# Kernel tuning notes

Measured on AMD Instinct MI355X. Metric: run time of the kernel, lower is better.

The kernel has to match this reference:

```python
import jax, jax.numpy as jnp
import numpy as np
from jax import lax

T, S, H, A = 1024, 1024, 2048, 128


def setup_inputs() -> dict:
    key = jax.random.key(0)
    ks = jax.random.split(key, 11)
    sc = 0.02  # small init scale to keep gates in a reasonable range
    rn = lambda k, shp: jax.random.normal(k, shp, dtype=jnp.float32) * sc
    return {
        "x": jax.random.normal(ks[0], (T, S), dtype=jnp.float32),
        "W_ih1": rn(ks[1], (4 * H, S)),
        "W_hh1": rn(ks[2], (4 * H, H)),
        "b_ih1": rn(ks[3], (4 * H,)),
        "b_hh1": rn(ks[4], (4 * H,)),
        "W_ih2": rn(ks[5], (4 * H, H)),
        "W_hh2": rn(ks[6], (4 * H, H)),
        "b_ih2": rn(ks[7], (4 * H,)),
        "b_hh2": rn(ks[8], (4 * H,)),
        "W_lin": rn(ks[9], (A, H)),
        "b_lin": rn(ks[10], (A,)),
    }


def _lstm_cell(xt, h, c, W_ih, W_hh, b):
    # PyTorch LSTMCell: gates ordered (i, f, g, o)
    gates = xt @ W_ih.T + h @ W_hh.T + b  # [4H]
    i, f, g, o = jnp.split(gates, 4)
    c_new = jax.nn.sigmoid(f) * c + jax.nn.sigmoid(i) * jnp.tanh(g)
    h_new = jax.nn.sigmoid(o) * jnp.tanh(c_new)
    return h_new, c_new


def reference(x, W_ih1, W_hh1, b_ih1, b_hh1, W_ih2, W_hh2, b_ih2, b_hh2, W_lin, b_lin):
    Hd = W_hh1.shape[1]
    b1 = b_ih1 + b_hh1
    b2 = b_ih2 + b_hh2

    def step(carry, xt):
        h1, c1, h2, c2 = carry
        h1, c1 = _lstm_cell(xt, h1, c1, W_ih1, W_hh1, b1)
        h2, c2 = _lstm_cell(h1, h2, c2, W_ih2, W_hh2, b2)
        return (h1, c1, h2, c2), None

    z = jnp.zeros((Hd,), dtype=x.dtype)
    (h1, c1, h2, c2), _ = lax.scan(step, (z, z, z, z), x)
    # linear head on final h of layer 2; batch==1 so [-1] == the single row
    return h2 @ W_lin.T + b_lin  # [A]
```

## Files before the change

kernel.cpp:

```cpp
#include <hip/hip_runtime.h>

#define T_ 1024
#define S_ 1024
#define H_ 2048
#define A_ 128
#define NBLK 256
#define THR 256

typedef __attribute__((ext_vector_type(8))) short short8;
typedef __attribute__((ext_vector_type(4))) float f32x4;

__device__ __forceinline__ float sigmf(float v) { return 1.0f / (1.0f + __expf(-v)); }

__device__ __forceinline__ ushort f2bf(float f) {
    uint u = __float_as_uint(f);
    return (ushort)((u + 0x7fffu + ((u >> 16) & 1u)) >> 16);
}

__device__ __forceinline__ short8 pack8(const float* __restrict__ s) {
    const float4 f0 = *(const float4*)(s);
    const float4 f1 = *(const float4*)(s + 4);
    uint4 o;
    o.x = (uint)f2bf(f0.x) | ((uint)f2bf(f0.y) << 16);
    o.y = (uint)f2bf(f0.z) | ((uint)f2bf(f0.w) << 16);
    o.z = (uint)f2bf(f1.x) | ((uint)f2bf(f1.y) << 16);
    o.w = (uint)f2bf(f1.z) | ((uint)f2bf(f1.w) << 16);
    return __builtin_bit_cast(short8, o);
}

__device__ __forceinline__ void poll8(const uint* __restrict__ p, uint tag, uint* g) {
    for (;;) {
#pragma unroll
        for (int i = 0; i < 8; ++i)
            g[i] = __hip_atomic_load(p + i, __ATOMIC_RELAXED, __HIP_MEMORY_SCOPE_AGENT);
        uint bad = 0;
#pragma unroll
        for (int i = 0; i < 8; ++i) bad |= (g[i] >> 16) ^ tag;
        if (bad == 0) return;
        __builtin_amdgcn_s_sleep(1);
    }
}

__device__ __forceinline__ void pack_hc(const uint* g, ushort* dst) {
    uint4 o;
    o.x = (g[0] & 0xffffu) | (g[1] << 16); o.y = (g[2] & 0xffffu) | (g[3] << 16);
    o.z = (g[4] & 0xffffu) | (g[5] << 16); o.w = (g[6] & 0xffffu) | (g[7] << 16);
    *(uint4*)dst = o;
}

__global__ void cvt_bf16(const float* __restrict__ src,
                         ushort* __restrict__ dst, int n4) {
    int i = blockIdx.x * blockDim.x + threadIdx.x;
    const int stride = gridDim.x * blockDim.x;
    for (; i < n4; i += stride) {
        const uint4 u = reinterpret_cast<const uint4*>(src)[i];
        ushort4 o;
        uint a;
        a = u.x; o.x = (ushort)((a + 0x7fffu + ((a >> 16) & 1u)) >> 16);
        a = u.y; o.y = (ushort)((a + 0x7fffu + ((a >> 16) & 1u)) >> 16);
        a = u.z; o.z = (ushort)((a + 0x7fffu + ((a >> 16) & 1u)) >> 16);
        a = u.w; o.w = (ushort)((a + 0x7fffu + ((a >> 16) & 1u)) >> 16);
        reinterpret_cast<ushort4*>(dst)[i] = o;
    }
}

__global__ __launch_bounds__(256, 2) void gemm_x1(
    const ushort* __restrict__ Abf, const ushort* __restrict__ Bbf,
    const float* __restrict__ bih1, const float* __restrict__ bhh1,
    float* __restrict__ X1) {
    __shared__ ushort At[64][80];
    __shared__ ushort Bt[64][80];
    const int tx = threadIdx.x;
    const int w = tx >> 6, lane = tx & 63;
    const int row0 = blockIdx.x * 64;
    const int col0 = blockIdx.y * 64;
    f32x4 acc[4];
#pragma unroll
    for (int n4 = 0; n4 < 4; ++n4) { acc[n4][0] = 0.f; acc[n4][1] = 0.f; acc[n4][2] = 0.f; acc[n4][3] = 0.f; }
    const int sr = tx >> 2, sc = (tx & 3) * 16;
    for (int k0 = 0; k0 < 1024; k0 += 64) {
        const uint4 a0 = *(const uint4*)(Abf + (size_t)(row0 + sr) * 1024 + k0 + sc);
        const uint4 a1 = *(const uint4*)(Abf + (size_t)(row0 + sr) * 1024 + k0 + sc + 8);
        const uint4 b0 = *(const uint4*)(Bbf + (size_t)(col0 + sr) * 1024 + k0 + sc);
        const uint4 b1 = *(const uint4*)(Bbf + (size_t)(col0 + sr) * 1024 + k0 + sc + 8);
        __syncthreads();
        *(uint4*)(&At[sr][sc]) = a0;
        *(uint4*)(&At[sr][sc + 8]) = a1;
        *(uint4*)(&Bt[sr][sc]) = b0;
        *(uint4*)(&Bt[sr][sc + 8]) = b1;
        __syncthreads();
#pragma unroll
        for (int kk = 0; kk < 64; kk += 32) {
            short8 af = *(const short8*)(&At[16 * w + (lane & 15)][kk + (lane >> 4) * 8]);
#pragma unroll
            for (int n4 = 0; n4 < 4; ++n4) {
                short8 bf = *(const short8*)(&Bt[n4 * 16 + (lane & 15)][kk + (lane >> 4) * 8]);
                acc[n4] = __builtin_amdgcn_mfma_f32_16x16x32_bf16(af, bf, acc[n4], 0, 0, 0);
            }
        }
    }
#pragma unroll
    for (int n4 = 0; n4 < 4; ++n4) {
        const int col = col0 + n4 * 16 + (lane & 15);
        const float bias = bih1[col] + bhh1[col];
#pragma unroll
        for (int r = 0; r < 4; ++r) {
            const int rowv = row0 + 16 * w + (lane >> 4) * 4 + r;
            X1[(size_t)rowv * 8192 + col] = acc[n4][r] + bias;
        }
    }
}

__global__ __launch_bounds__(THR, 1) void lstm_mfma(
    const float* __restrict__ X1,
    const float* __restrict__ Whh1,
    const float* __restrict__ W2i, const float* __restrict__ W2h,
    const float* __restrict__ bih2, const float* __restrict__ bhh2,
    const float* __restrict__ Wlin, const float* __restrict__ blin,
    uint* __restrict__ hp1, uint* __restrict__ hp2,
    float* __restrict__ out)
{
    __shared__ ushort hc[4096];
    __shared__ float pl[4][64];

    const int b = blockIdx.x, tid = threadIdx.x;
    const int w = tid >> 6, lane = tid & 63;
    const int j0 = b * 8;
    const int m = lane & 15;
    const int ko = (lane >> 4) * 8;

    short8 a1[2][16];
#pragma unroll
    for (int g = 0; g < 2; ++g) {
        const int r = g * 16 + m;
        const int R = (r & 3) * H_ + j0 + (r >> 2);
        const float* src = Whh1 + (size_t)R * H_ + w * 512 + ko;
#pragma unroll
        for (int c = 0; c < 16; ++c)
            a1[g][c] = pack8(src + c * 32);
    }
    short8 a2[2][32];
#pragma unroll
    for (int g = 0; g < 2; ++g) {
        const int r = g * 16 + m;
        const int R = (r & 3) * H_ + j0 + (r >> 2);
        const float* base = (w < 2) ? (W2i + (size_t)R * H_ + w * 1024 + ko)
                                    : (W2h + (size_t)R * H_ + (w - 2) * 1024 + ko);
#pragma unroll
        for (int c = 0; c < 32; ++c)
            a2[g][c] = pack8(base + c * 32);
    }

    float c1 = 0.f, c2 = 0.f;
    float b2g[4] = {0.f, 0.f, 0.f, 0.f};
    if (tid >= 8 && tid < 16) {
        const int jl = tid - 8;
#pragma unroll
        for (int g = 0; g < 4; ++g) {
            const int R = g * H_ + j0 + jl;
            b2g[g] = bih2[R] + bhh2[R];
        }
    }

#pragma unroll 1
    for (int t = 0; t <= T_; ++t) {
        float xg[4] = {0.f, 0.f, 0.f, 0.f};
        if (tid < 8 && t < T_) {
#pragma unroll
            for (int g = 0; g < 4; ++g)
                xg[g] = X1[(size_t)t * 8192 + g * H_ + j0 + tid];
        }

        {
            uint g0[8];
            if (t >= 1) {
                const uint* p = hp1 + ((((t - 1) & 1) * 256 + tid) << 4);
                poll8(p, (uint)(t - 1) & 0xffffu, g0);
            } else {
#pragma unroll
                for (int i = 0; i < 8; ++i) g0[i] = 0u;
            }
            pack_hc(g0, hc + tid * 8);
        }
        __syncthreads();

        if (t < T_) {
            f32x4 acc0, acc1;
#pragma unroll
            for (int r = 0; r < 4; ++r) { acc0[r] = 0.f; acc1[r] = 0.f; }
            const ushort* h1s = hc + w * 512;
#pragma unroll
            for (int c = 0; c < 16; ++c) {
                const short8 bfr = *(const short8*)(h1s + c * 32 + ko);
                acc0 = __builtin_amdgcn_mfma_f32_16x16x32_bf16(a1[0][c], bfr, acc0, 0, 0, 0);
                acc1 = __builtin_amdgcn_mfma_f32_16x16x32_bf16(a1[1][c], bfr, acc1, 0, 0, 0);
            }
            if (m == 0) {
                const int r4 = (lane >> 4) * 4;
#pragma unroll
                for (int r = 0; r < 4; ++r) {
                    pl[w][ 0 + r4 + r] = acc0[r];
                    pl[w][16 + r4 + r] = acc1[r];
                }
            }
        }
        __syncthreads();

        if (tid < 8 && t < T_) {
            float s[4];
#pragma unroll
            for (int g = 0; g < 4; ++g)
                s[g] = pl[0][tid * 4 + g] + pl[1][tid * 4 + g]
                     + pl[2][tid * 4 + g] + pl[3][tid * 4 + g];
            const float ig = sigmf(s[0] + xg[0]);
            const float fg = sigmf(s[1] + xg[1]);
            const float gv = tanhf(s[2] + xg[2]);
            const float og = sigmf(s[3] + xg[3]);
            c1 = fg * c1 + ig * gv;
            const float h1n = og * tanhf(c1);
            const uint pv = (((uint)t & 0xffffu) << 16) | (uint)f2bf(h1n);
            __hip_atomic_store(hp1 + (((t & 1) * 256 + b) << 4) + tid, pv,
                               __ATOMIC_RELAXED, __HIP_MEMORY_SCOPE_AGENT);
        }

        {
            uint g1[8];
            if (t >= 2) {
                const uint* p = hp2 + ((((t - 2) & 1) * 256 + tid) << 4);
                poll8(p, (uint)(t - 2) & 0xffffu, g1);
            } else {
#pragma unroll
                for (int i = 0; i < 8; ++i) g1[i] = 0u;
            }
            pack_hc(g1, hc + 2048 + tid * 8);
        }
        __syncthreads();

        if (t >= 1) {
            f32x4 acc2, acc3;
#pragma unroll
            for (int r = 0; r < 4; ++r) { acc2[r] = 0.f; acc3[r] = 0.f; }
            const ushort* hcs = hc + w * 1024;
#pragma unroll
            for (int c = 0; c < 32; ++c) {
                const short8 bfr = *(const short8*)(hcs + c * 32 + ko);
                acc2 = __builtin_amdgcn_mfma_f32_16x16x32_bf16(a2[0][c], bfr, acc2, 0, 0, 0);
                acc3 = __builtin_amdgcn_mfma_f32_16x16x32_bf16(a2[1][c], bfr, acc3, 0, 0, 0);
            }
            if (m == 0) {
                const int r4 = (lane >> 4) * 4;
#pragma unroll
                for (int r = 0; r < 4; ++r) {
                    pl[w][32 + r4 + r] = acc2[r];
                    pl[w][48 + r4 + r] = acc3[r];
                }
            }
        }
        __syncthreads();

        if (tid >= 8 && tid < 16 && t >= 1) {
            const int jl = tid - 8;
            float s2[4];
#pragma unroll
            for (int g = 0; g < 4; ++g)
                s2[g] = pl[0][32 + jl * 4 + g] + pl[1][32 + jl * 4 + g]
                      + pl[2][32 + jl * 4 + g] + pl[3][32 + jl * 4 + g];
            const float ig = sigmf(s2[0] + b2g[0]);
            const float fg = sigmf(s2[1] + b2g[1]);
            const float gv = tanhf(s2[2] + b2g[2]);
            const float og = sigmf(s2[3] + b2g[3]);
            c2 = fg * c2 + ig * gv;
            const float h2n = og * tanhf(c2);
            const int s = t - 1;
            const uint pv = (((uint)s & 0xffffu) << 16) | (uint)f2bf(h2n);
            __hip_atomic_store(hp2 + (((s & 1) * 256 + b) << 4) + jl, pv,
                               __ATOMIC_RELAXED, __HIP_MEMORY_SCOPE_AGENT);
        }
    }

    if (b < 16) {
        __syncthreads();
        {
            uint gg[8];
            const uint* p = hp2 + (((((T_ - 1) & 1)) * 256 + tid) << 4);
            poll8(p, (uint)(T_ - 1) & 0xffffu, gg);
            pack_hc(gg, hc + tid * 8);
        }
        __syncthreads();
#pragma unroll
        for (int rr = 0; rr < 2; ++rr) {
            const int r = b * 8 + w * 2 + rr;
            const float* wrow = Wlin + (size_t)r * H_;
            float a = 0.f;
#pragma unroll
            for (int p4 = 0; p4 < 4; ++p4) {
                const int o8 = p4 * 512 + lane * 8;
                const uint4 hq = *(const uint4*)(hc + o8);
                float hv[8];
                hv[0] = __uint_as_float(hq.x << 16); hv[1] = __uint_as_float(hq.x & 0xffff0000u);
                hv[2] = __uint_as_float(hq.y << 16); hv[3] = __uint_as_float(hq.y & 0xffff0000u);
                hv[4] = __uint_as_float(hq.z << 16); hv[5] = __uint_as_float(hq.z & 0xffff0000u);
                hv[6] = __uint_as_float(hq.w << 16); hv[7] = __uint_as_float(hq.w & 0xffff0000u);
                const float4 w0 = *(const float4*)(wrow + o8);
                const float4 w1v = *(const float4*)(wrow + o8 + 4);
                a = fmaf(w0.x, hv[0], a); a = fmaf(w0.y, hv[1], a);
                a = fmaf(w0.z, hv[2], a); a = fmaf(w0.w, hv[3], a);
                a = fmaf(w1v.x, hv[4], a); a = fmaf(w1v.y, hv[5], a);
                a = fmaf(w1v.z, hv[6], a); a = fmaf(w1v.w, hv[7], a);
            }
#pragma unroll
            for (int off = 1; off < 64; off <<= 1) a += __shfl_xor(a, off);
            if (lane == 0) out[r] = a + blin[r];
        }
    }
}

extern "C" void kernel_launch(void* const* d_in, const int* in_sizes, int n_in,
                              void* d_out, int out_size, void* d_ws, size_t ws_size,
                              hipStream_t stream) {
    const float* x    = (const float*)d_in[0];
    const float* Wih1 = (const float*)d_in[1];
    const float* Whh1 = (const float*)d_in[2];
    const float* bih1 = (const float*)d_in[3];
    const float* bhh1 = (const float*)d_in[4];
    const float* Wih2 = (const float*)d_in[5];
    const float* Whh2 = (const float*)d_in[6];
    const float* bih2 = (const float*)d_in[7];
    const float* bhh2 = (const float*)d_in[8];
    const float* Wlin = (const float*)d_in[9];
    const float* blin = (const float*)d_in[10];
    float* out = (float*)d_out;

    float*  X1    = (float*)d_ws;
    ushort* xbf   = (ushort*)((char*)d_ws + 33554432);
    ushort* w1ibf = (ushort*)((char*)d_ws + 35651584);
    uint*   hp1   = (uint*)((char*)d_ws + 52428800);
    uint*   hp2   = (uint*)((char*)d_ws + 52461568);

    hipLaunchKernelGGL(cvt_bf16, dim3(512), dim3(256), 0, stream, x, xbf, 262144);
    hipLaunchKernelGGL(cvt_bf16, dim3(2048), dim3(256), 0, stream, Wih1, w1ibf, 2097152);
    hipLaunchKernelGGL(gemm_x1, dim3(16, 128), dim3(256), 0, stream,
                       (const ushort*)xbf, (const ushort*)w1ibf, bih1, bhh1, X1);
    hipMemsetAsync((void*)hp1, 0xFF, 65536, stream);

    hipLaunchKernelGGL(lstm_mfma, dim3(NBLK), dim3(THR), 0, stream,
                       X1, Whh1, Wih2, Whh2, bih2, bhh2, Wlin, blin,
                       hp1, hp2, out);
}
```

Measured before the change: 5.502 ms.

## Prefetch inter-block h flags early and verify later to hide polling latency

Splits the polling of hidden-state flags into an early speculative load and a later verify-and-retry step. The next layer-1 h values are prefetched at the end of each step, and the layer-2 h loads are issued before the layer-1 MFMA work and checked after it, which also removes one __syncthreads per timestep. The aim is to overlap global atomic-load latency on the recurrent critical path with compute. Speculative loads that arrive too early fall back to re-polling, so each stale read adds a sleep-and-reload round.

```diff
diff --git a/kernel.cpp b/kernel.cpp
--- a/kernel.cpp
+++ b/kernel.cpp
@@ -28,17 +28,24 @@
     return __builtin_bit_cast(short8, o);
 }
 
-__device__ __forceinline__ void poll8(const uint* __restrict__ p, uint tag, uint* g) {
+__device__ __forceinline__ void verify8(const uint* __restrict__ p, uint tag, uint* g) {
     for (;;) {
-#pragma unroll
-        for (int i = 0; i < 8; ++i)
-            g[i] = __hip_atomic_load(p + i, __ATOMIC_RELAXED, __HIP_MEMORY_SCOPE_AGENT);
         uint bad = 0;
 #pragma unroll
         for (int i = 0; i < 8; ++i) bad |= (g[i] >> 16) ^ tag;
         if (bad == 0) return;
         __builtin_amdgcn_s_sleep(1);
-    }
+#pragma unroll
+        for (int i = 0; i < 8; ++i)
+            g[i] = __hip_atomic_load(p + i, __ATOMIC_RELAXED, __HIP_MEMORY_SCOPE_AGENT);
+    }
+}
+
+__device__ __forceinline__ void poll8(const uint* __restrict__ p, uint tag, uint* g) {
+#pragma unroll
+    for (int i = 0; i < 8; ++i)
+        g[i] = __hip_atomic_load(p + i, __ATOMIC_RELAXED, __HIP_MEMORY_SCOPE_AGENT);
+    verify8(p, tag, g);
 }
 
 __device__ __forceinline__ void pack_hc(const uint* g, ushort* dst) {
@@ -162,6 +169,10 @@
         }
     }
 
+    uint g0n[8];
+#pragma unroll
+    for (int i = 0; i < 8; ++i) g0n[i] = 0u;
+
 #pragma unroll 1
     for (int t = 0; t <= T_; ++t) {
         float xg[4] = {0.f, 0.f, 0.f, 0.f};
@@ -171,16 +182,21 @@
                 xg[g] = X1[(size_t)t * 8192 + g * H_ + j0 + tid];
         }
 
-        {
-            uint g0[8];
-            if (t >= 1) {
-                const uint* p = hp1 + ((((t - 1) & 1) * 256 + tid) << 4);
-                poll8(p, (uint)(t - 1) & 0xffffu, g0);
-            } else {
-#pragma unroll
-                for (int i = 0; i < 8; ++i) g0[i] = 0u;
-            }
-            pack_hc(g0, hc + tid * 8);
+        if (t >= 1) {
+            const uint* p = hp1 + ((((t - 1) & 1) * 256 + tid) << 4);
+            verify8(p, (uint)(t - 1) & 0xffffu, g0n);
+        }
+        pack_hc(g0n, hc + tid * 8);
+
+        uint g1[8];
+        if (t >= 2) {
+            const uint* p2 = hp2 + ((((t - 2) & 1) * 256 + tid) << 4);
+#pragma unroll
+            for (int i = 0; i < 8; ++i)
+                g1[i] = __hip_atomic_load(p2 + i, __ATOMIC_RELAXED, __HIP_MEMORY_SCOPE_AGENT);
+        } else {
+#pragma unroll
+            for (int i = 0; i < 8; ++i) g1[i] = 0u;
         }
         __syncthreads();
 
@@ -204,6 +220,12 @@
                 }
             }
         }
+
+        if (t >= 2) {
+            const uint* p2 = hp2 + ((((t - 2) & 1) * 256 + tid) << 4);
+            verify8(p2, (uint)(t - 2) & 0xffffu, g1);
+        }
+        pack_hc(g1, hc + 2048 + tid * 8);
         __syncthreads();
 
         if (tid < 8 && t < T_) {
@@ -222,19 +244,6 @@
             __hip_atomic_store(hp1 + (((t & 1) * 256 + b) << 4) + tid, pv,
                                __ATOMIC_RELAXED, __HIP_MEMORY_SCOPE_AGENT);
         }
-
-        {
-            uint g1[8];
-            if (t >= 2) {
-                const uint* p = hp2 + ((((t - 2) & 1) * 256 + tid) << 4);
-                poll8(p, (uint)(t - 2) & 0xffffu, g1);
-            } else {
-#pragma unroll
-                for (int i = 0; i < 8; ++i) g1[i] = 0u;
-            }
-            pack_hc(g1, hc + 2048 + tid * 8);
-        }
-        __syncthreads();
 
         if (t >= 1) {
             f32x4 acc2, acc3;
@@ -275,6 +284,13 @@
             const uint pv = (((uint)s & 0xffffu) << 16) | (uint)f2bf(h2n);
             __hip_atomic_store(hp2 + (((s & 1) * 256 + b) << 4) + jl, pv,
                                __ATOMIC_RELAXED, __HIP_MEMORY_SCOPE_AGENT);
+        }
+
+        if (t < T_) {
+            const uint* pn = hp1 + (((t & 1) * 256 + tid) << 4);
+#pragma unroll
+            for (int i = 0; i < 8; ++i)
+                g0n[i] = __hip_atomic_load(pn + i, __ATOMIC_RELAXED, __HIP_MEMORY_SCOPE_AGENT);
         }
     }
 
```

Measured after the change: 4.894 ms (median of 2 runs). 1.12x faster.

## Give each wave its own h slice and prefetch h vectors to cut block barriers

Applied to the files above, without the earlier changes.

Each wave now polls and unpacks only the slice of the hidden-state vectors that its own MFMA loop reads, into separate LDS buffers. This removes the two block-wide barriers per timestep that used to follow the shared h staging. The polls use 64-bit atomic loads. Layer-2 h loads are issued before the layer-1 compute, and the next step's h1 is loaded speculatively at the end of each iteration, to hide global-memory latency on the serial recurrence. The cost is more register pressure and redundant re-polling when the speculative loads see stale tags.

```diff
diff --git a/kernel.cpp b/kernel.cpp
--- a/kernel.cpp
+++ b/kernel.cpp
@@ -9,6 +9,7 @@
 
 typedef __attribute__((ext_vector_type(8))) short short8;
 typedef __attribute__((ext_vector_type(4))) float f32x4;
+typedef unsigned long long u64;
 
 __device__ __forceinline__ float sigmf(float v) { return 1.0f / (1.0f + __expf(-v)); }
 
@@ -28,6 +29,40 @@
     return __builtin_bit_cast(short8, o);
 }
 
+__device__ __forceinline__ u64 ldq(const u64* p) {
+    return __hip_atomic_load(p, __ATOMIC_RELAXED, __HIP_MEMORY_SCOPE_AGENT);
+}
+__device__ __forceinline__ uint pay32(u64 v) {
+    return (uint)(v & 0xffffu) | (((uint)(v >> 32)) << 16);
+}
+
+__device__ __forceinline__ void verify4(const u64* __restrict__ p, uint tag, u64* v) {
+    const u64 rep = ((u64)tag << 16) | ((u64)tag << 48);
+    for (;;) {
+        u64 bad = 0;
+#pragma unroll
+        for (int i = 0; i < 4; ++i) bad |= (v[i] ^ rep) & 0xffff0000ffff0000ull;
+        if (bad == 0) return;
+        __builtin_amdgcn_s_sleep(1);
+#pragma unroll
+        for (int i = 0; i < 4; ++i) v[i] = ldq(p + i);
+    }
+}
+__device__ __forceinline__ void verify8q(const u64* __restrict__ p, uint tag, u64* v) {
+    const u64 rep = ((u64)tag << 16) | ((u64)tag << 48);
+    for (;;) {
+        u64 bad = 0;
+#pragma unroll
+        for (int i = 0; i < 8; ++i) bad |= (v[i] ^ rep) & 0xffff0000ffff0000ull;
+        if (bad == 0) return;
+        __builtin_amdgcn_s_sleep(1);
+#pragma unroll
+        for (int i = 0; i < 4; ++i) v[i] = ldq(p + i);
+#pragma unroll
+        for (int i = 0; i < 4; ++i) v[4 + i] = ldq(p + 8 + i);
+    }
+}
+
 __device__ __forceinline__ void poll8(const uint* __restrict__ p, uint tag, uint* g) {
     for (;;) {
 #pragma unroll
@@ -39,13 +74,6 @@
         if (bad == 0) return;
         __builtin_amdgcn_s_sleep(1);
     }
-}
-
-__device__ __forceinline__ void pack_hc(const uint* g, ushort* dst) {
-    uint4 o;
-    o.x = (g[0] & 0xffffu) | (g[1] << 16); o.y = (g[2] & 0xffffu) | (g[3] << 16);
-    o.z = (g[4] & 0xffffu) | (g[5] << 16); o.w = (g[6] & 0xffffu) | (g[7] << 16);
-    *(uint4*)dst = o;
 }
 
 __global__ void cvt_bf16(const float* __restrict__ src,
@@ -120,7 +148,8 @@
     uint* __restrict__ hp1, uint* __restrict__ hp2,
     float* __restrict__ out)
 {
-    __shared__ ushort hc[4096];
+    __shared__ ushort hcA[2048];
+    __shared__ ushort hcB[4096];
     __shared__ float pl[4][64];
 
     const int b = blockIdx.x, tid = threadIdx.x;
@@ -162,6 +191,13 @@
         }
     }
 
+    const u64* hq1 = (const u64*)hp1;
+    const u64* hq2 = (const u64*)hp2;
+    const bool l2h1 = (w < 2);
+    const int  l2ln = (l2h1 ? w : (w - 2)) * 128 + 2 * lane;
+
+    u64 pre[4] = {0ull, 0ull, 0ull, 0ull};
+
 #pragma unroll 1
     for (int t = 0; t <= T_; ++t) {
         float xg[4] = {0.f, 0.f, 0.f, 0.f};
@@ -171,24 +207,36 @@
                 xg[g] = X1[(size_t)t * 8192 + g * H_ + j0 + tid];
         }
 
+        const bool needL2 = l2h1 ? (t >= 1) : (t >= 2);
+        const int  l2slot = l2h1 ? ((t - 1) & 1) : (t & 1);
+        const u64* lp = (l2h1 ? hq1 : hq2) + ((size_t)(l2slot * 256 + l2ln) << 3);
+        u64 lv[8];
+        if (needL2) {
+#pragma unroll
+            for (int i = 0; i < 4; ++i) lv[i] = ldq(lp + i);
+#pragma unroll
+            for (int i = 0; i < 4; ++i) lv[4 + i] = ldq(lp + 8 + i);
+        } else {
+#pragma unroll
+            for (int i = 0; i < 8; ++i) lv[i] = 0ull;
+        }
+
+        if (t >= 1) {
+            const u64* pp = hq1 + ((size_t)((((t - 1) & 1)) * 256 + w * 64 + lane) << 3);
+            verify4(pp, (uint)(t - 1) & 0xffffu, pre);
+        }
         {
-            uint g0[8];
-            if (t >= 1) {
-                const uint* p = hp1 + ((((t - 1) & 1) * 256 + tid) << 4);
-                poll8(p, (uint)(t - 1) & 0xffffu, g0);
-            } else {
-#pragma unroll
-                for (int i = 0; i < 8; ++i) g0[i] = 0u;
-            }
-            pack_hc(g0, hc + tid * 8);
-        }
-        __syncthreads();
+            uint4 o;
+            o.x = pay32(pre[0]); o.y = pay32(pre[1]);
+            o.z = pay32(pre[2]); o.w = pay32(pre[3]);
+            *(uint4*)(hcA + w * 512 + lane * 8) = o;
+        }
 
         if (t < T_) {
             f32x4 acc0, acc1;
 #pragma unroll
             for (int r = 0; r < 4; ++r) { acc0[r] = 0.f; acc1[r] = 0.f; }
-            const ushort* h1s = hc + w * 512;
+            const ushort* h1s = hcA + w * 512;
 #pragma unroll
             for (int c = 0; c < 16; ++c) {
                 const short8 bfr = *(const short8*)(h1s + c * 32 + ko);
@@ -223,24 +271,23 @@
                                __ATOMIC_RELAXED, __HIP_MEMORY_SCOPE_AGENT);
         }
 
+        if (needL2) {
+            verify8q(lp, (uint)(l2h1 ? (t - 1) : (t - 2)) & 0xffffu, lv);
+        }
         {
-            uint g1[8];
-            if (t >= 2) {
-                const uint* p = hp2 + ((((t - 2) & 1) * 256 + tid) << 4);
-                poll8(p, (uint)(t - 2) & 0xffffu, g1);
-            } else {
-#pragma unroll
-                for (int i = 0; i < 8; ++i) g1[i] = 0u;
-            }
-            pack_hc(g1, hc + 2048 + tid * 8);
-        }
-        __syncthreads();
-
+            uint4 o0, o1;
+            o0.x = pay32(lv[0]); o0.y = pay32(lv[1]);
+            o0.z = pay32(lv[2]); o0.w = pay32(lv[3]);
+            o1.x = pay32(lv[4]); o1.y = pay32(lv[5]);
+            o1.z = pay32(lv[6]); o1.w = pay32(lv[7]);
+            *(uint4*)(hcB + w * 1024 + lane * 16) = o0;
+            *(uint4*)(hcB + w * 1024 + lane * 16 + 8) = o1;
+        }
         if (t >= 1) {
             f32x4 acc2, acc3;
 #pragma unroll
             for (int r = 0; r < 4; ++r) { acc2[r] = 0.f; acc3[r] = 0.f; }
-            const ushort* hcs = hc + w * 1024;
+            const ushort* hcs = hcB + w * 1024;
 #pragma unroll
             for (int c = 0; c < 32; ++c) {
                 const short8 bfr = *(const short8*)(hcs + c * 32 + ko);
@@ -276,6 +323,12 @@
             __hip_atomic_store(hp2 + (((s & 1) * 256 + b) << 4) + jl, pv,
                                __ATOMIC_RELAXED, __HIP_MEMORY_SCOPE_AGENT);
         }
+
+        if (t < T_) {
+            const u64* pn = hq1 + ((size_t)((t & 1) * 256 + w * 64 + lane) << 3);
+#pragma unroll
+            for (int i = 0; i < 4; ++i) pre[i] = ldq(pn + i);
+        }
     }
 
     if (b < 16) {
@@ -284,7 +337,12 @@
             uint gg[8];
             const uint* p = hp2 + (((((T_ - 1) & 1)) * 256 + tid) << 4);
             poll8(p, (uint)(T_ - 1) & 0xffffu, gg);
-            pack_hc(gg, hc + tid * 8);
+            uint4 o;
+            o.x = (gg[0] & 0xffffu) | (gg[1] << 16);
+            o.y = (gg[2] & 0xffffu) | (gg[3] << 16);
+            o.z = (gg[4] & 0xffffu) | (gg[5] << 16);
+            o.w = (gg[6] & 0xffffu) | (gg[7] << 16);
+            *(uint4*)(hcA + ((tid & 127) * 8) + ((tid >> 7) * 1024)) = o;
         }
         __syncthreads();
 #pragma unroll
@@ -295,7 +353,7 @@
 #pragma unroll
             for (int p4 = 0; p4 < 4; ++p4) {
                 const int o8 = p4 * 512 + lane * 8;
-                const uint4 hq = *(const uint4*)(hc + o8);
+                const uint4 hq = *(const uint4*)(hcA + o8);
                 float hv[8];
                 hv[0] = __uint_as_float(hq.x << 16); hv[1] = __uint_as_float(hq.x & 0xffff0000u);
                 hv[2] = __uint_as_float(hq.y << 16); hv[3] = __uint_as_float(hq.y & 0xffff0000u);
```

New measurement: 8.509 ms. +54.7%, slower.
